# Kernel tuning notes

Measured on AMD Instinct MI355X. Metric: run time of the kernel, lower is better.

## Reference

```python
import jax, jax.numpy as jnp
import numpy as np

STEPS = 32768
D_IO = 63      # input/output feature size (hardcoded in module)
H = 256        # hidden_size
L = 6          # num_layers


def setup_inputs() -> dict:
    key = jax.random.key(0)
    ks = jax.random.split(key, 9)
    s = 1.0 / np.sqrt(H)
    inputs = jax.random.normal(ks[0], (STEPS, D_IO), dtype=jnp.float32)
    W_in = jax.random.uniform(ks[1], (H, D_IO), minval=-s, maxval=s, dtype=jnp.float32)
    b_in = jax.random.uniform(ks[2], (H,), minval=-s, maxval=s, dtype=jnp.float32)
    # PyTorch LSTM weights: per layer W_ih [4H, in], W_hh [4H, H], biases [4H].
    # Layer 0 input size == H (after the input Linear), so all layers share shape.
    W_ih = jax.random.uniform(ks[3], (L, 4 * H, H), minval=-s, maxval=s, dtype=jnp.float32)
    W_hh = jax.random.uniform(ks[4], (L, 4 * H, H), minval=-s, maxval=s, dtype=jnp.float32)
    b_ih = jax.random.uniform(ks[5], (L, 4 * H), minval=-s, maxval=s, dtype=jnp.float32)
    b_hh = jax.random.uniform(ks[6], (L, 4 * H), minval=-s, maxval=s, dtype=jnp.float32)
    W_fc = jax.random.uniform(ks[7], (D_IO, H), minval=-s, maxval=s, dtype=jnp.float32)
    b_fc = jax.random.uniform(ks[8], (D_IO,), minval=-s, maxval=s, dtype=jnp.float32)
    return {"inputs": inputs, "W_in": W_in, "b_in": b_in, "W_ih": W_ih,
            "W_hh": W_hh, "b_ih": b_ih, "b_hh": b_hh, "W_fc": W_fc, "b_fc": b_fc}


def _forward(inputs, W_in, b_in, W_ih, W_hh, b_ih, b_hh, W_fc, b_fc):
    # Original forward calls step(input, None) each timestep -> hidden state is
    # reset to zeros every step, so all timesteps are independent and can be
    # batched along the step axis.
    x = inputs @ W_in.T + b_in  # (S, H)
    h = x
    for l in range(L):
        h_prev = jnp.zeros_like(h)  # zero initial hidden state each step
        # gates: (S, 4H); h_prev @ W_hh kept for math-faithfulness to cuDNN step
        gates = h @ W_ih[l].T + h_prev @ W_hh[l].T + b_ih[l] + b_hh[l]
        i, f, g, o = jnp.split(gates, 4, axis=-1)  # torch gate order i,f,g,o
        c = jax.nn.sigmoid(i) * jnp.tanh(g)        # f * c_prev == 0
        h = jax.nn.sigmoid(o) * jnp.tanh(c)
    out = h @ W_fc.T + b_fc  # (S, 63)
    # matches the `outputs` buffer of shape (steps, 1, 63)
    return out[:, None, :]


def reference(inputs, W_in, b_in, W_ih, W_hh, b_ih, b_hh, W_fc, b_fc):
    return _forward(inputs, W_in, b_in, W_ih, W_hh, b_ih, b_hh, W_fc, b_fc)
```

## Files before the change

kernel.cpp:

```cpp
#include <hip/hip_runtime.h>

#define STEPS 32768
#define DIO 63
#define HSZ 256
#define NL 6
#define BM 64
#define THREADS 512

#define NBGF  (NL * 2 * 8 * 8 * 3 * 512)
#define NBIAS (NL * 768)
#define NBINF (16 * 2 * 64 * 8)
#define NBFCF (4 * 8 * 64 * 8)

typedef __bf16 bf16_8 __attribute__((ext_vector_type(8)));
typedef __bf16 bf16_4 __attribute__((ext_vector_type(4)));
typedef float f32x4 __attribute__((ext_vector_type(4)));

#define LOG2E  1.4426950408889634f
#define LOG2E2 2.8853900817779268f

__device__ __forceinline__ unsigned short f2bf(float f) {
    unsigned int u = __float_as_uint(f);
    u = u + 0x7fffu + ((u >> 16) & 1u);
    return (unsigned short)(u >> 16);
}

__global__ void prep_kernel(const float* __restrict__ W_in,
                            const float* __restrict__ W_ih,
                            const float* __restrict__ b_ih,
                            const float* __restrict__ b_hh,
                            const float* __restrict__ W_fc,
                            unsigned short* __restrict__ Bg,
                            float* __restrict__ bias,
                            unsigned short* __restrict__ Bin,
                            unsigned short* __restrict__ Bfc) {
    int idx = blockIdx.x * 256 + threadIdx.x;
    if (idx < NBGF) {
        int e    = idx & 7;
        int lane = (idx >> 3) & 63;
        int t    = idx >> 9;
        int g    = t % 3;
        int u    = t / 3;
        int kk   = u & 7;
        int v    = u >> 3;
        int w    = v & 7;
        int x    = v >> 3;
        int p    = x & 1;
        int l    = x >> 1;
        int f = (p * 8 + w) * 16 + (lane & 15);
        int k = kk * 32 + (lane >> 4) * 8 + e;
        int r = f + (g == 0 ? 0 : (g == 1 ? 512 : 768));
        float sc = (g == 1) ? LOG2E2 : LOG2E;
        Bg[idx] = f2bf(W_ih[((size_t)l * 1024 + r) * HSZ + k] * sc);
        return;
    }
    idx -= NBGF;
    if (idx < NBIAS) {
        int j = idx % 768, l = idx / 768;
        int g = j >> 8;
        int r = (j < 256) ? j : j + 256;
        float sc = (g == 1) ? LOG2E2 : LOG2E;
        bias[idx] = (b_ih[l * 1024 + r] + b_hh[l * 1024 + r]) * sc;
        return;
    }
    idx -= NBIAS;
    if (idx < NBINF) {
        int e = idx & 7, lane = (idx >> 3) & 63, kk = (idx >> 9) & 1, fb = idx >> 10;
        int f = fb * 16 + (lane & 15);
        int k = kk * 32 + (lane >> 4) * 8 + e;
        Bin[idx] = (k < DIO) ? f2bf(W_in[f * DIO + k]) : (unsigned short)0;
        return;
    }
    idx -= NBINF;
    if (idx < NBFCF) {
        int e = idx & 7, lane = (idx >> 3) & 63, kk = (idx >> 9) & 7, fm = idx >> 12;
        int f = fm * 16 + (lane & 15);
        int k = kk * 32 + (lane >> 4) * 8 + e;
        Bfc[idx] = (f < DIO) ? f2bf(W_fc[f * HSZ + k]) : (unsigned short)0;
    }
}

__device__ __forceinline__ void ld3(const char* p, bf16_8& a, bf16_8& g, bf16_8& o) {
    a = *(const bf16_8*)(p);
    g = *(const bf16_8*)(p + 1024);
    o = *(const bf16_8*)(p + 2048);
}

__device__ __forceinline__ void gate_pass(
    const char* pW, const char* pNext,
    bf16_8& wa0, bf16_8& wg0, bf16_8& wo0,
    const char* cur, int rdB, const float* pb,
    f32x4 (&ai)[4], f32x4 (&ag)[4], f32x4 (&ao)[4]) {
    f32x4 bi4 = *(const f32x4*)(pb);
    f32x4 bg4 = *(const f32x4*)(pb + 256);
    f32x4 bo4 = *(const f32x4*)(pb + 512);
#pragma unroll
    for (int n = 0; n < 4; ++n) { ai[n] = bi4; ag[n] = bg4; ao[n] = bo4; }
    bf16_8 wa = wa0, wg = wg0, wo = wo0;
#pragma unroll
    for (int kk = 0; kk < 8; ++kk) {
        bf16_8 na, ng, no;
        if (kk < 7) ld3(pW + (kk + 1) * 3072, na, ng, no);
        else        ld3(pNext, na, ng, no);
        bf16_8 b[4];
#pragma unroll
        for (int n = 0; n < 4; ++n)
            b[n] = *(const bf16_8*)(cur + rdB + kk * 4096 + n * 256);
#pragma unroll
        for (int n = 0; n < 4; ++n) {
            ai[n] = __builtin_amdgcn_mfma_f32_16x16x32_bf16(wa, b[n], ai[n], 0, 0, 0);
            ag[n] = __builtin_amdgcn_mfma_f32_16x16x32_bf16(wg, b[n], ag[n], 0, 0, 0);
            ao[n] = __builtin_amdgcn_mfma_f32_16x16x32_bf16(wo, b[n], ao[n], 0, 0, 0);
        }
        wa = na; wg = ng; wo = no;
    }
    wa0 = wa; wg0 = wg; wo0 = wo;
}

__device__ __forceinline__ void act_write(char* nxt, int fb, int lq, int l15,
                                          f32x4 (&ai)[4], f32x4 (&ag)[4], f32x4 (&ao)[4]) {
    const int wrp = (fb >> 1) * 4096 + ((fb & 1) * 2 + (lq >> 1)) * 1024 +
                    l15 * 16 + (lq & 1) * 8;
#pragma unroll
    for (int n = 0; n < 4; ++n) {
        bf16_4 hv;
#pragma unroll
        for (int r = 0; r < 4; ++r) {
            float ei = __builtin_amdgcn_exp2f(ai[n][r]);
            float eg = __builtin_amdgcn_exp2f(ag[n][r]);
            float eo = __builtin_amdgcn_exp2f(ao[n][r]);
            float c = ei * (eg - 1.f) *
                      __builtin_amdgcn_rcpf((1.f + ei) * (1.f + eg));
            float z = c * c;
            hv[r] = (__bf16)(eo * c * (z + 15.f) *
                             __builtin_amdgcn_rcpf((1.f + eo) * fmaf(6.f, z, 15.f)));
        }
        *(bf16_4*)(nxt + wrp + n * 256) = hv;
    }
}

__global__ __launch_bounds__(THREADS, 2) void rnn_fused(
    const float* __restrict__ inp, const float* __restrict__ b_in,
    const float* __restrict__ b_fc,
    const unsigned short* __restrict__ Bg, const float* __restrict__ bias,
    const unsigned short* __restrict__ Bin, const unsigned short* __restrict__ Bfc,
    float* __restrict__ out) {
    __shared__ __align__(16) unsigned short h_lds[2 * 8 * 4 * 64 * 8];
    unsigned short* in_alias = h_lds + 16384;

    const int tid = threadIdx.x;
    const int lane = tid & 63;
    const int l15 = lane & 15;
    const int lq = lane >> 4;
    const int wid = tid >> 6;
    const int row0 = blockIdx.x * BM;
    const int rdB = lq * 1024 + l15 * 16;

    const char* Wb = (const char*)Bg + lane * 16;
    const int pA = wid & 1, pB = 1 - pA;

    bf16_8 wa0, wg0, wo0;
    ld3(Wb + (size_t)(pA * 8 + wid) * 24576, wa0, wg0, wo0);

    for (int idx = tid; idx < BM * 64; idx += THREADS) {
        int s = idx >> 6, k = idx & 63;
        float v = (k < DIO) ? inp[(size_t)(row0 + s) * DIO + k] : 0.f;
        int off = (k >> 5) * 4096 + ((k >> 3) & 3) * 1024 + s * 16 + (k & 7) * 2;
        *(unsigned short*)((char*)in_alias + off) = f2bf(v);
    }
    __syncthreads();

    {
        f32x4 acc[2][4];
#pragma unroll
        for (int m = 0; m < 2; ++m) {
            f32x4 b4 = *(const f32x4*)(b_in + (2 * wid + m) * 16 + lq * 4);
#pragma unroll
            for (int n = 0; n < 4; ++n) acc[m][n] = b4;
        }
        const bf16_8* __restrict__ pIA = (const bf16_8*)Bin + lane;
#pragma unroll
        for (int kk = 0; kk < 2; ++kk) {
            bf16_8 a[2], b[4];
#pragma unroll
            for (int m = 0; m < 2; ++m) a[m] = pIA[((2 * wid + m) * 2 + kk) * 64];
#pragma unroll
            for (int n = 0; n < 4; ++n)
                b[n] = *(const bf16_8*)((const char*)in_alias + rdB + kk * 4096 + n * 256);
#pragma unroll
            for (int m = 0; m < 2; ++m)
#pragma unroll
                for (int n = 0; n < 4; ++n)
                    acc[m][n] = __builtin_amdgcn_mfma_f32_16x16x32_bf16(a[m], b[n], acc[m][n], 0, 0, 0);
        }
#pragma unroll
        for (int m = 0; m < 2; ++m) {
            int wb = wid * 4096 + (2 * m + (lq >> 1)) * 1024 + l15 * 16 + (lq & 1) * 8;
#pragma unroll
            for (int n = 0; n < 4; ++n) {
                bf16_4 hv;
#pragma unroll
                for (int r = 0; r < 4; ++r) hv[r] = (__bf16)acc[m][n][r];
                *(bf16_4*)((char*)h_lds + wb + n * 256) = hv;
            }
        }
    }
    __syncthreads();

    for (int l = 0; l < NL; ++l) {
        const char* cur = (const char*)h_lds + (l & 1) * 32768;
        char* nxt = (char*)h_lds + ((l + 1) & 1) * 32768;
        const char* pWA = Wb + (size_t)((l * 2 + pA) * 8 + wid) * 24576;
        const char* pWB = Wb + (size_t)((l * 2 + pB) * 8 + wid) * 24576;
        const char* pWN = (l < NL - 1)
            ? Wb + (size_t)(((l + 1) * 2 + pA) * 8 + wid) * 24576
            : pWB;
        const float* bl = bias + l * 768 + lq * 4;

        f32x4 ai[4], ag[4], ao[4];
        gate_pass(pWA, pWB, wa0, wg0, wo0, cur, rdB,
                  bl + (pA * 8 + wid) * 16, ai, ag, ao);
        act_write(nxt, pA * 8 + wid, lq, l15, ai, ag, ao);
        gate_pass(pWB, pWN, wa0, wg0, wo0, cur, rdB,
                  bl + (pB * 8 + wid) * 16, ai, ag, ao);
        act_write(nxt, pB * 8 + wid, lq, l15, ai, ag, ao);
        __syncthreads();
    }

    {
        const char* cur = (const char*)h_lds;
        const int fm = wid & 3;
        const int sb = (wid >> 2) * 2;
        f32x4 o4[2];
#pragma unroll
        for (int n = 0; n < 2; ++n) o4[n] = (f32x4){0.f, 0.f, 0.f, 0.f};
        const bf16_8* __restrict__ pF = (const bf16_8*)Bfc + lane;
#pragma unroll
        for (int kk = 0; kk < 8; ++kk) {
            bf16_8 a = pF[(fm * 8 + kk) * 64];
#pragma unroll
            for (int n = 0; n < 2; ++n) {
                bf16_8 b = *(const bf16_8*)(cur + rdB + kk * 4096 + (sb + n) * 256);
                o4[n] = __builtin_amdgcn_mfma_f32_16x16x32_bf16(a, b, o4[n], 0, 0, 0);
            }
        }
#pragma unroll
        for (int n = 0; n < 2; ++n) {
            int s = row0 + (sb + n) * 16 + l15;
#pragma unroll
            for (int r = 0; r < 4; ++r) {
                int f = fm * 16 + lq * 4 + r;
                if (f < DIO) out[(size_t)s * DIO + f] = o4[n][r] + b_fc[f];
            }
        }
    }
}

extern "C" void kernel_launch(void* const* d_in, const int* in_sizes, int n_in,
                              void* d_out, int out_size, void* d_ws, size_t ws_size,
                              hipStream_t stream) {
    const float* inputs = (const float*)d_in[0];
    const float* W_in   = (const float*)d_in[1];
    const float* b_in   = (const float*)d_in[2];
    const float* W_ih   = (const float*)d_in[3];
    const float* b_ih   = (const float*)d_in[5];
    const float* b_hh   = (const float*)d_in[6];
    const float* W_fc   = (const float*)d_in[7];
    const float* b_fc   = (const float*)d_in[8];

    unsigned short* Bg  = (unsigned short*)d_ws;
    float* bias         = (float*)((char*)d_ws + (size_t)NBGF * 2);
    unsigned short* Bin = (unsigned short*)((char*)bias + (size_t)NBIAS * 4);
    unsigned short* Bfc = Bin + NBINF;

    int total = NBGF + NBIAS + NBINF + NBFCF;
    prep_kernel<<<(total + 255) / 256, 256, 0, stream>>>(W_in, W_ih, b_ih, b_hh, W_fc,
                                                         Bg, bias, Bin, Bfc);
    rnn_fused<<<STEPS / BM, THREADS, 0, stream>>>(inputs, b_in, b_fc, Bg, bias, Bin, Bfc,
                                                  (float*)d_out);
}
```

Baseline: 115.2 us.

## Use 16 waves per block, one feature block per wave, drop weight prefetch

Doubles the block to 1024 threads so each of 16 waves computes one 16-feature gate block per layer instead of two sequential passes. The input projection and FC epilogue are re-split across the 16 waves, and the weight layout in prep is simplified to match. The cross-pass software prefetch of weights is removed, so weight global loads are no longer overlapped explicitly. Launch bounds now request 4 blocks per CU, which tightens the register budget.

New measurement: 99.45 us (median of 2 runs). -13.7%, faster.

```diff
diff --git a/kernel.cpp b/kernel.cpp
--- a/kernel.cpp
+++ b/kernel.cpp
@@ -5,9 +5,9 @@
 #define HSZ 256
 #define NL 6
 #define BM 64
-#define THREADS 512
-
-#define NBGF  (NL * 2 * 8 * 8 * 3 * 512)
+#define THREADS 1024
+
+#define NBGF  (NL * 16 * 8 * 3 * 512)
 #define NBIAS (NL * 768)
 #define NBINF (16 * 2 * 64 * 8)
 #define NBFCF (4 * 8 * 64 * 8)
@@ -43,11 +43,9 @@
         int u    = t / 3;
         int kk   = u & 7;
         int v    = u >> 3;
-        int w    = v & 7;
-        int x    = v >> 3;
-        int p    = x & 1;
-        int l    = x >> 1;
-        int f = (p * 8 + w) * 16 + (lane & 15);
+        int w    = v & 15;
+        int l    = v >> 4;
+        int f = w * 16 + (lane & 15);
         int k = kk * 32 + (lane >> 4) * 8 + e;
         int r = f + (g == 0 ? 0 : (g == 1 ? 512 : 768));
         float sc = (g == 1) ? LOG2E2 : LOG2E;
@@ -73,48 +71,11 @@
     }
     idx -= NBINF;
     if (idx < NBFCF) {
-        int e = idx & 7, lane = (idx >> 3) & 63, kk = (idx >> 9) & 7, fm = idx >> 12;
-        int f = fm * 16 + (lane & 15);
+        int e = idx & 7, lane = (idx >> 3) & 63, kk = (idx >> 9) & 7, ff = idx >> 12;
+        int f = ff * 16 + (lane & 15);
         int k = kk * 32 + (lane >> 4) * 8 + e;
         Bfc[idx] = (f < DIO) ? f2bf(W_fc[f * HSZ + k]) : (unsigned short)0;
     }
-}
-
-__device__ __forceinline__ void ld3(const char* p, bf16_8& a, bf16_8& g, bf16_8& o) {
-    a = *(const bf16_8*)(p);
-    g = *(const bf16_8*)(p + 1024);
-    o = *(const bf16_8*)(p + 2048);
-}
-
-__device__ __forceinline__ void gate_pass(
-    const char* pW, const char* pNext,
-    bf16_8& wa0, bf16_8& wg0, bf16_8& wo0,
-    const char* cur, int rdB, const float* pb,
-    f32x4 (&ai)[4], f32x4 (&ag)[4], f32x4 (&ao)[4]) {
-    f32x4 bi4 = *(const f32x4*)(pb);
-    f32x4 bg4 = *(const f32x4*)(pb + 256);
-    f32x4 bo4 = *(const f32x4*)(pb + 512);
-#pragma unroll
-    for (int n = 0; n < 4; ++n) { ai[n] = bi4; ag[n] = bg4; ao[n] = bo4; }
-    bf16_8 wa = wa0, wg = wg0, wo = wo0;
-#pragma unroll
-    for (int kk = 0; kk < 8; ++kk) {
-        bf16_8 na, ng, no;
-        if (kk < 7) ld3(pW + (kk + 1) * 3072, na, ng, no);
-        else        ld3(pNext, na, ng, no);
-        bf16_8 b[4];
-#pragma unroll
-        for (int n = 0; n < 4; ++n)
-            b[n] = *(const bf16_8*)(cur + rdB + kk * 4096 + n * 256);
-#pragma unroll
-        for (int n = 0; n < 4; ++n) {
-            ai[n] = __builtin_amdgcn_mfma_f32_16x16x32_bf16(wa, b[n], ai[n], 0, 0, 0);
-            ag[n] = __builtin_amdgcn_mfma_f32_16x16x32_bf16(wg, b[n], ag[n], 0, 0, 0);
-            ao[n] = __builtin_amdgcn_mfma_f32_16x16x32_bf16(wo, b[n], ao[n], 0, 0, 0);
-        }
-        wa = na; wg = ng; wo = no;
-    }
-    wa0 = wa; wg0 = wg; wo0 = wo;
 }
 
 __device__ __forceinline__ void act_write(char* nxt, int fb, int lq, int l15,
@@ -139,7 +100,7 @@
     }
 }
 
-__global__ __launch_bounds__(THREADS, 2) void rnn_fused(
+__global__ __launch_bounds__(THREADS, 4) void rnn_fused(
     const float* __restrict__ inp, const float* __restrict__ b_in,
     const float* __restrict__ b_fc,
     const unsigned short* __restrict__ Bg, const float* __restrict__ bias,
@@ -156,12 +117,6 @@
     const int row0 = blockIdx.x * BM;
     const int rdB = lq * 1024 + l15 * 16;
 
-    const char* Wb = (const char*)Bg + lane * 16;
-    const int pA = wid & 1, pB = 1 - pA;
-
-    bf16_8 wa0, wg0, wo0;
-    ld3(Wb + (size_t)(pA * 8 + wid) * 24576, wa0, wg0, wo0);
-
     for (int idx = tid; idx < BM * 64; idx += THREADS) {
         int s = idx >> 6, k = idx & 63;
         float v = (k < DIO) ? inp[(size_t)(row0 + s) * DIO + k] : 0.f;
@@ -171,87 +126,86 @@
     __syncthreads();
 
     {
-        f32x4 acc[2][4];
-#pragma unroll
-        for (int m = 0; m < 2; ++m) {
-            f32x4 b4 = *(const f32x4*)(b_in + (2 * wid + m) * 16 + lq * 4);
-#pragma unroll
-            for (int n = 0; n < 4; ++n) acc[m][n] = b4;
+        f32x4 acc[4];
+        {
+            f32x4 b4 = *(const f32x4*)(b_in + wid * 16 + lq * 4);
+#pragma unroll
+            for (int n = 0; n < 4; ++n) acc[n] = b4;
         }
         const bf16_8* __restrict__ pIA = (const bf16_8*)Bin + lane;
 #pragma unroll
         for (int kk = 0; kk < 2; ++kk) {
-            bf16_8 a[2], b[4];
-#pragma unroll
-            for (int m = 0; m < 2; ++m) a[m] = pIA[((2 * wid + m) * 2 + kk) * 64];
-#pragma unroll
-            for (int n = 0; n < 4; ++n)
-                b[n] = *(const bf16_8*)((const char*)in_alias + rdB + kk * 4096 + n * 256);
-#pragma unroll
-            for (int m = 0; m < 2; ++m)
-#pragma unroll
-                for (int n = 0; n < 4; ++n)
-                    acc[m][n] = __builtin_amdgcn_mfma_f32_16x16x32_bf16(a[m], b[n], acc[m][n], 0, 0, 0);
-        }
-#pragma unroll
-        for (int m = 0; m < 2; ++m) {
-            int wb = wid * 4096 + (2 * m + (lq >> 1)) * 1024 + l15 * 16 + (lq & 1) * 8;
+            bf16_8 a = pIA[(wid * 2 + kk) * 64];
 #pragma unroll
             for (int n = 0; n < 4; ++n) {
-                bf16_4 hv;
-#pragma unroll
-                for (int r = 0; r < 4; ++r) hv[r] = (__bf16)acc[m][n][r];
-                *(bf16_4*)((char*)h_lds + wb + n * 256) = hv;
+                bf16_8 b = *(const bf16_8*)((const char*)in_alias + rdB + kk * 4096 + n * 256);
+                acc[n] = __builtin_amdgcn_mfma_f32_16x16x32_bf16(a, b, acc[n], 0, 0, 0);
             }
         }
+        const int wrp = (wid >> 1) * 4096 + ((wid & 1) * 2 + (lq >> 1)) * 1024 +
+                        l15 * 16 + (lq & 1) * 8;
+#pragma unroll
+        for (int n = 0; n < 4; ++n) {
+            bf16_4 hv;
+#pragma unroll
+            for (int r = 0; r < 4; ++r) hv[r] = (__bf16)acc[n][r];
+            *(bf16_4*)((char*)h_lds + wrp + n * 256) = hv;
+        }
     }
     __syncthreads();
 
+    const char* Wb = (const char*)Bg + lane * 16;
     for (int l = 0; l < NL; ++l) {
         const char* cur = (const char*)h_lds + (l & 1) * 32768;
         char* nxt = (char*)h_lds + ((l + 1) & 1) * 32768;
-        const char* pWA = Wb + (size_t)((l * 2 + pA) * 8 + wid) * 24576;
-        const char* pWB = Wb + (size_t)((l * 2 + pB) * 8 + wid) * 24576;
-        const char* pWN = (l < NL - 1)
-            ? Wb + (size_t)(((l + 1) * 2 + pA) * 8 + wid) * 24576
-            : pWB;
-        const float* bl = bias + l * 768 + lq * 4;
+        const char* pW = Wb + (size_t)(l * 16 + wid) * 24576;
+        const float* pb = bias + l * 768 + wid * 16 + lq * 4;
 
         f32x4 ai[4], ag[4], ao[4];
-        gate_pass(pWA, pWB, wa0, wg0, wo0, cur, rdB,
-                  bl + (pA * 8 + wid) * 16, ai, ag, ao);
-        act_write(nxt, pA * 8 + wid, lq, l15, ai, ag, ao);
-        gate_pass(pWB, pWN, wa0, wg0, wo0, cur, rdB,
-                  bl + (pB * 8 + wid) * 16, ai, ag, ao);
-        act_write(nxt, pB * 8 + wid, lq, l15, ai, ag, ao);
+        {
+            f32x4 bi4 = *(const f32x4*)(pb);
+            f32x4 bg4 = *(const f32x4*)(pb + 256);
+            f32x4 bo4 = *(const f32x4*)(pb + 512);
+#pragma unroll
+            for (int n = 0; n < 4; ++n) { ai[n] = bi4; ag[n] = bg4; ao[n] = bo4; }
+        }
+#pragma unroll
+        for (int kk = 0; kk < 8; ++kk) {
+            bf16_8 wa = *(const bf16_8*)(pW + kk * 3072);
+            bf16_8 wg = *(const bf16_8*)(pW + kk * 3072 + 1024);
+            bf16_8 wo = *(const bf16_8*)(pW + kk * 3072 + 2048);
+            bf16_8 b[4];
+#pragma unroll
+            for (int n = 0; n < 4; ++n)
+                b[n] = *(const bf16_8*)(cur + rdB + kk * 4096 + n * 256);
+#pragma unroll
+            for (int n = 0; n < 4; ++n) {
+                ai[n] = __builtin_amdgcn_mfma_f32_16x16x32_bf16(wa, b[n], ai[n], 0, 0, 0);
+                ag[n] = __builtin_amdgcn_mfma_f32_16x16x32_bf16(wg, b[n], ag[n], 0, 0, 0);
+                ao[n] = __builtin_amdgcn_mfma_f32_16x16x32_bf16(wo, b[n], ao[n], 0, 0, 0);
+            }
+        }
+        act_write(nxt, wid, lq, l15, ai, ag, ao);
         __syncthreads();
     }
 
     {
         const char* cur = (const char*)h_lds;
-        const int fm = wid & 3;
-        const int sb = (wid >> 2) * 2;
-        f32x4 o4[2];
-#pragma unroll
-        for (int n = 0; n < 2; ++n) o4[n] = (f32x4){0.f, 0.f, 0.f, 0.f};
+        const int ff = wid & 3;
+        const int sf = wid >> 2;
+        f32x4 o4 = (f32x4){0.f, 0.f, 0.f, 0.f};
         const bf16_8* __restrict__ pF = (const bf16_8*)Bfc + lane;
 #pragma unroll
         for (int kk = 0; kk < 8; ++kk) {
-            bf16_8 a = pF[(fm * 8 + kk) * 64];
-#pragma unroll
-            for (int n = 0; n < 2; ++n) {
-                bf16_8 b = *(const bf16_8*)(cur + rdB + kk * 4096 + (sb + n) * 256);
-                o4[n] = __builtin_amdgcn_mfma_f32_16x16x32_bf16(a, b, o4[n], 0, 0, 0);
-            }
-        }
-#pragma unroll
-        for (int n = 0; n < 2; ++n) {
-            int s = row0 + (sb + n) * 16 + l15;
-#pragma unroll
-            for (int r = 0; r < 4; ++r) {
-                int f = fm * 16 + lq * 4 + r;
-                if (f < DIO) out[(size_t)s * DIO + f] = o4[n][r] + b_fc[f];
-            }
+            bf16_8 a = pF[(ff * 8 + kk) * 64];
+            bf16_8 b = *(const bf16_8*)(cur + rdB + kk * 4096 + sf * 256);
+            o4 = __builtin_amdgcn_mfma_f32_16x16x32_bf16(a, b, o4, 0, 0, 0);
+        }
+        int s = row0 + sf * 16 + l15;
+#pragma unroll
+        for (int r = 0; r < 4; ++r) {
+            int f = ff * 16 + lq * 4 + r;
+            if (f < DIO) out[(size_t)s * DIO + f] = o4[r] + b_fc[f];
         }
     }
 }
```
